# Kernel optimization log

Measured on AMD Instinct MI355X. Metric: run time of the kernel, lower is better.

Reference implementation:

```python
import jax, jax.numpy as jnp
import numpy as np

MIN_NORM = 1e-15
BALL_EPS = 4e-3  # float32 proj eps used by HGCN PoincareBall
C_IN = 1.0
C_OUT = 1.0
N_NODES = 100000
N_EDGES = 1200000
DIM = 64
RATIO = 0.75


def _artanh(x):
    x = jnp.clip(x, -1.0 + 1e-7, 1.0 - 1e-7)
    return 0.5 * (jnp.log1p(x) - jnp.log1p(-x))


def _norm(x):
    return jnp.clip(jnp.linalg.norm(x, axis=-1, keepdims=True), MIN_NORM, None)


def proj(x, c):
    n = _norm(x)
    maxnorm = (1.0 - BALL_EPS) / jnp.sqrt(c)
    return jnp.where(n > maxnorm, x / n * maxnorm, x)


def expmap0(u, c):
    sc = jnp.sqrt(c)
    n = _norm(u)
    return jnp.tanh(sc * n) * u / (sc * n)


def logmap0(p, c):
    sc = jnp.sqrt(c)
    n = _norm(p)
    return _artanh(sc * n) * p / (sc * n)


def mobius_add(x, y, c):
    x2 = jnp.sum(x * x, -1, keepdims=True)
    y2 = jnp.sum(y * y, -1, keepdims=True)
    xy = jnp.sum(x * y, -1, keepdims=True)
    num = (1.0 + 2.0 * c * xy + c * y2) * x + (1.0 - c * x2) * y
    den = 1.0 + 2.0 * c * xy + c * c * x2 * y2
    return num / jnp.clip(den, MIN_NORM, None)


def mobius_matvec(m, x, c):
    sc = jnp.sqrt(c)
    xn = _norm(x)
    mx = x @ m.T  # [N, out]
    mxn = _norm(mx)
    res = jnp.tanh(mxn / xn * _artanh(sc * xn)) * mx / (mxn * sc)
    zero = jnp.all(mx == 0, axis=-1, keepdims=True)
    return jnp.where(zero, jnp.zeros((), mx.dtype), res)


def setup_inputs() -> dict:
    key = jax.random.key(0)
    k1, k2, k3, k4 = jax.random.split(key, 4)
    # points on the Poincare ball (small tangent vectors exp-mapped)
    x = proj(expmap0(0.01 * jax.random.normal(k1, (N_NODES, DIM), jnp.float32), C_IN), C_IN)
    edge_index = jax.random.randint(k2, (2, N_EDGES), 0, N_NODES, dtype=jnp.int32)
    xav = float(np.sqrt(2.0) * np.sqrt(6.0 / (DIM + DIM)))  # xavier_uniform gain sqrt(2) scale
    weight = jax.random.uniform(k3, (DIM, DIM), jnp.float32, -xav, xav)
    bias = jnp.zeros((DIM,), jnp.float32)
    lw_w = jax.random.normal(k4, (1, 2 * DIM), jnp.float32) * 0.05
    lw_b = jnp.zeros((1,), jnp.float32)
    return {"x": x, "edge_index": edge_index, "weight": weight, "bias": bias, "lw_w": lw_w, "lw_b": lw_b}


def reference(x, edge_index, weight, bias, lw_w, lw_b):
    N = x.shape[0]
    # ---- HypLinear (eval mode, dropout=0) ----
    h = proj(mobius_matvec(weight, x, C_IN), C_IN)
    hyp_bias = proj(expmap0(bias[None, :], C_IN), C_IN)  # proj_tan0 is identity on Poincare ball
    h = proj(mobius_add(h, hyp_bias, C_IN), C_IN)
    # ---- NodeSelect ----
    x_tan = logmap0(h, C_IN)  # [N, D]
    src, dst = edge_index[0], edge_index[1]
    agg = lambda v: jax.ops.segment_sum(v[src], dst, num_segments=N)  # scatter-add over edges
    sum_neigh = agg(x_tan)
    # NodeInformationScore: (I - D^{-1/2} A D^{-1/2}) x with self-loops removed from A
    w = (src != dst).astype(x_tan.dtype)
    deg = jax.ops.segment_sum(w, src, num_segments=N)
    dinv = jnp.where(deg > 0, deg ** -0.5, 0.0)
    norm_w = -(dinv[src] * w * dinv[dst])  # [E]
    info = x_tan + jax.ops.segment_sum(norm_w[:, None] * x_tan[src], dst, num_segments=N)
    score = jnp.sum(jnp.abs(info), axis=1)  # [N]
    k = int(N * RATIO)
    top_vals, _ = jax.lax.top_k(score, k)
    T = top_vals[k - 1]  # min of top-k
    sel = (score > T).astype(x_tan.dtype)[:, None]  # hot_prob mask [N,1]
    sum_sel = agg(sel * x_tan)
    gate = jax.nn.sigmoid(jnp.concatenate([sum_sel, sum_neigh], axis=-1) @ lw_w.T + lw_b)  # [N,1]
    a_x = jax.nn.relu(agg(gate * sel * x_tan))
    out = x_tan + a_x
    out = proj(expmap0(out, C_IN), C_IN)
    # ---- HypAct (relu) ----
    out = jax.nn.relu(out)
    out = proj(expmap0(out, C_OUT), C_OUT)
    return out
```

## Files before the change

kernel.cpp:

```cpp
#include <hip/hip_runtime.h>
#include <math.h>


#define MAXN_D 0.996
#define MAXN_F 0.996f
#define NPB 64
#define GPT 512
#define NBMAX 512
#define BCAP 6144
#define BINBLK 256
#define SELB 128
#define SBIN 8192
#define CAND_CAP 16384

typedef unsigned long long ull;

__device__ __forceinline__ double wsumd(double v){
#pragma unroll
  for(int o=32;o;o>>=1) v += __shfl_xor(v,o,64);
  return v;
}
__device__ __forceinline__ float wsumf(float v){
#pragma unroll
  for(int o=32;o;o>>=1) v += __shfl_xor(v,o,64);
  return v;
}
__device__ __forceinline__ double qsumd(double v){
#pragma unroll
  for(int o=1;o<16;o<<=1) v += __shfl_xor(v,o,64);
  return v;
}
__device__ __forceinline__ float qsumf(float v){
#pragma unroll
  for(int o=1;o<16;o<<=1) v += __shfl_xor(v,o,64);
  return v;
}
__device__ __forceinline__ double gsumd(double v){
  v += __shfl_xor(v,16,64); v += __shfl_xor(v,32,64); return v;
}
__device__ __forceinline__ float gsumf(float v){
  v += __shfl_xor(v,16,64); v += __shfl_xor(v,32,64); return v;
}

__global__ __launch_bounds__(256) void k_init(
    const float* __restrict__ bias, double* __restrict__ hb,
    double* __restrict__ hb2, int* __restrict__ rem, int kth,
    int* __restrict__ dstCur, int* __restrict__ srcCur, int NB){
  if(threadIdx.x < 64){
    int lane = threadIdx.x;
    double b = (double)bias[lane];
    double n = fmax(sqrt(wsumd(b*b)), 1e-15);
    double e = tanh(n)*b/n;
    double en = fmax(sqrt(wsumd(e*e)), 1e-15);
    if(en > MAXN_D) e *= MAXN_D/en;
    hb[lane] = e;
    double s2 = wsumd(e*e);
    if(lane==0) *hb2 = s2;
  }
  if(threadIdx.x == 0) *rem = kth;
  for(int b=threadIdx.x; b<NB; b+=256){
    dstCur[b] = b*BCAP;
    srcCur[b] = b*BCAP;
  }
}

__global__ __launch_bounds__(256) void k_binPlace(const int* __restrict__ ei, int E,
    int NB, int chunk, int* __restrict__ dstCur, int* __restrict__ srcCur,
    ull* __restrict__ dstbin, int* __restrict__ srcbin){
  __shared__ int dh[NBMAX], sh_[NBMAX];
  __shared__ int db[NBMAX], sb[NBMAX];
  for(int t=threadIdx.x; t<NB; t+=256){ dh[t]=0; sh_[t]=0; }
  __syncthreads();
  int start = blockIdx.x*chunk, end = min(E, start+chunk);
  for(int e=start+(int)threadIdx.x; e<end; e+=256){
    int s = ei[e], d = ei[(size_t)E+e];
    atomicAdd(&dh[d>>8],1);
    if(s!=d) atomicAdd(&sh_[s>>8],1);
  }
  __syncthreads();
  for(int t=threadIdx.x; t<NB; t+=256){
    db[t] = dh[t]  ? atomicAdd(&dstCur[t], dh[t])  : 0;
    sb[t] = sh_[t] ? atomicAdd(&srcCur[t], sh_[t]) : 0;
  }
  __syncthreads();
  for(int t=threadIdx.x; t<NB; t+=256){ dh[t]=db[t]; sh_[t]=sb[t]; }
  __syncthreads();
  for(int e=start+(int)threadIdx.x; e<end; e+=256){
    int s = ei[e], d = ei[(size_t)E+e];
    int p = atomicAdd(&dh[d>>8],1);
    dstbin[p] = ((ull)(unsigned)d<<32) | (unsigned)s;
    if(s!=d){ int p2 = atomicAdd(&sh_[s>>8],1); srcbin[p2] = s; }
  }
}

__global__ __launch_bounds__(256) void k_bucketAB(
    const ull* __restrict__ dstbin, const int* __restrict__ dstCur,
    int* __restrict__ rowbeg, int* __restrict__ rowcnt, int* __restrict__ csr,
    const int* __restrict__ srcbin, const int* __restrict__ srcCur,
    double* __restrict__ dinv, int N){
  int b = blockIdx.x;
  int node0 = b<<8;
  int nodes = min(256, N-node0);
  __shared__ int c[256], ex[256];
  int t = threadIdx.x;
  {
    int base = b*BCAP, cnt = dstCur[b]-base;
    c[t]=0; __syncthreads();
    for(int e=base+t; e<base+cnt; e+=256){
      int d = (int)(dstbin[e]>>32);
      atomicAdd(&c[d-node0],1);
    }
    __syncthreads();
    int v = c[t]; ex[t]=v; __syncthreads();
    for(int off=1; off<256; off<<=1){
      int a = (t>=off) ? ex[t-off] : 0; __syncthreads();
      ex[t] += a; __syncthreads();
    }
    int mybase = base + ex[t] - v;
    if(t<nodes){ rowbeg[node0+t] = mybase; rowcnt[node0+t] = v; }
    c[t] = mybase;
    __syncthreads();
    for(int e=base+t; e<base+cnt; e+=256){
      ull pr = dstbin[e];
      int d = (int)(pr>>32);
      int p = atomicAdd(&c[d-node0],1);
      csr[p] = (int)(pr & 0xffffffffu);
    }
  }
  __syncthreads();
  {
    int base = b*BCAP, cnt = srcCur[b]-base;
    c[t]=0; __syncthreads();
    for(int e=base+t; e<base+cnt; e+=256)
      atomicAdd(&c[srcbin[e]-node0],1);
    __syncthreads();
    if(t<nodes){ int d = c[t]; dinv[node0+t] = (d>0) ? 1.0/sqrt((double)d) : 0.0; }
  }
}

__global__ __launch_bounds__(GPT) void k_gemmprep(
    const float* __restrict__ x, const float* __restrict__ W,
    const double* __restrict__ hb, const double* __restrict__ hb2p,
    const float* __restrict__ lww,
    double* __restrict__ xtd, float* __restrict__ xtf,
    float2* __restrict__ pab, int N){
  __shared__ float wf[4096];
  __shared__ float xf[NPB*64];
  __shared__ double r123[NPB][3];
  __shared__ double abuf[NPB][2];
  int tid = threadIdx.x;
  for(int a=tid; a<4096; a+=GPT){
    int j = (a>>2)&63;
    int k = ((a>>8)<<2) | (a&3);
    wf[a] = W[j*64 + k];
  }
  int i0 = blockIdx.x*NPB;
  for(int idx=tid; idx<NPB*64; idx+=GPT){
    int node = i0 + (idx>>6);
    xf[idx] = (node<N) ? x[(size_t)node*64 + (idx&63)] : 0.f;
  }
  __syncthreads();
  int lane = tid & 63;
  int nb = (tid>>6)*8;
  double acc0=0.0, acc1=0.0, acc2=0.0, acc3=0.0;
  double acc4=0.0, acc5=0.0, acc6=0.0, acc7=0.0;
  const float4* wq = (const float4*)wf;
  const float4* xq = (const float4*)xf;
#pragma unroll 2
  for(int k4=0; k4<16; ++k4){
    float4 w4 = wq[k4*64 + lane];
    double w0=(double)w4.x, w1=(double)w4.y, w2d=(double)w4.z, w3=(double)w4.w;
#define MAC(n, accn) { float4 v = xq[(nb+(n))*16 + k4];                       \
    accn = fma(w0,(double)v.x,accn); accn = fma(w1,(double)v.y,accn);         \
    accn = fma(w2d,(double)v.z,accn); accn = fma(w3,(double)v.w,accn); }
    MAC(0,acc0) MAC(1,acc1) MAC(2,acc2) MAC(3,acc3)
    MAC(4,acc4) MAC(5,acc5) MAC(6,acc6) MAC(7,acc7)
#undef MAC
  }
  double hbl = hb[lane];
#define RED4(A0,A1,A2,A3, OFF) {                                              \
    double xd0 = (double)xf[(nb+(OFF)+0)*64+lane];                            \
    double xd1 = (double)xf[(nb+(OFF)+1)*64+lane];                            \
    double xd2 = (double)xf[(nb+(OFF)+2)*64+lane];                            \
    double xd3 = (double)xf[(nb+(OFF)+3)*64+lane];                            \
    double s1_0 = wsumd(xd0*xd0), s2_0 = wsumd((A0)*(A0)), s3_0 = wsumd((A0)*hbl); \
    double s1_1 = wsumd(xd1*xd1), s2_1 = wsumd((A1)*(A1)), s3_1 = wsumd((A1)*hbl); \
    double s1_2 = wsumd(xd2*xd2), s2_2 = wsumd((A2)*(A2)), s3_2 = wsumd((A2)*hbl); \
    double s1_3 = wsumd(xd3*xd3), s2_3 = wsumd((A3)*(A3)), s3_3 = wsumd((A3)*hbl); \
    if(lane==0){                                                              \
      r123[nb+(OFF)+0][0]=s1_0; r123[nb+(OFF)+0][1]=s2_0; r123[nb+(OFF)+0][2]=s3_0; \
      r123[nb+(OFF)+1][0]=s1_1; r123[nb+(OFF)+1][1]=s2_1; r123[nb+(OFF)+1][2]=s3_1; \
      r123[nb+(OFF)+2][0]=s1_2; r123[nb+(OFF)+2][1]=s2_2; r123[nb+(OFF)+2][2]=s3_2; \
      r123[nb+(OFF)+3][0]=s1_3; r123[nb+(OFF)+3][1]=s2_3; r123[nb+(OFF)+3][2]=s3_3; \
    } }
  RED4(acc0,acc1,acc2,acc3, 0)
  RED4(acc4,acc5,acc6,acc7, 4)
#undef RED4
  __syncthreads();
  if(tid < 64){
    double x2s = r123[tid][0], m2 = r123[tid][1], mh = r123[tid][2];
    double y2 = *hb2p;
    double xn  = fmax(sqrt(x2s), 1e-15);
    double mxn = fmax(sqrt(m2), 1e-15);
    double xc  = fmin(fmax(xn, -1.0+1e-7), 1.0-1e-7);
    double at  = 0.5*(log1p(xc)-log1p(-xc));
    double f1  = tanh(mxn/xn*at)/mxn;
    if(m2 == 0.0) f1 = 0.0;
    double h2 = f1*f1*m2;
    double hn = fmax(sqrt(h2), 1e-15);
    if(hn > MAXN_D){ double s = MAXN_D/hn; f1 *= s; h2 = f1*f1*m2; }
    double xy = f1*mh;
    double den = fmax(1.0 + 2.0*xy + h2*y2, 1e-15);
    double a = (1.0 + 2.0*xy + y2)/den;
    double bb = (1.0 - h2)/den;
    double p2 = a*a*h2 + 2.0*a*bb*xy + bb*bb*y2;
    double pn = fmax(sqrt(p2), 1e-15);
    if(pn > MAXN_D){ double s = MAXN_D/pn; a*=s; bb*=s; pn = fmax(pn*s, 1e-15); }
    double nc  = fmin(fmax(pn, -1.0+1e-7), 1.0-1e-7);
    double at2 = 0.5*(log1p(nc)-log1p(-nc));
    double sc  = at2/pn;
    abuf[tid][0] = sc*a*f1;
    abuf[tid][1] = sc*bb;
  }
  __syncthreads();
  float wAl = lww[lane], wBl = lww[64+lane];
#define EMIT(n, accn) { int nd=i0+nb+(n); if(nd<N){                           \
    double al = abuf[nb+(n)][0], be = abuf[nb+(n)][1];                        \
    double v = al*(accn) + be*hbl;                                            \
    xtd[(size_t)nd*64+lane] = v;                                              \
    float vf = (float)v;                                                      \
    xtf[(size_t)nd*64+lane] = vf;                                             \
    float pA = wsumf(vf*wAl);                                                 \
    float pB = wsumf(vf*wBl);                                                 \
    if(lane==0) pab[nd] = make_float2(pA,pB); } }
  EMIT(0,acc0) EMIT(1,acc1) EMIT(2,acc2) EMIT(3,acc3)
  EMIT(4,acc4) EMIT(5,acc5) EMIT(6,acc6) EMIT(7,acc7)
#undef EMIT
}

__global__ void k_gatherA(const int* __restrict__ csr, const int* __restrict__ rowbeg,
                          const int* __restrict__ rowcnt,
                          const float* __restrict__ xtf, const double* __restrict__ xtd,
                          const double* __restrict__ dinv,
                          ull* __restrict__ keys, int N){
  int lane = threadIdx.x & 63;
  int i = (int)((blockIdx.x*(unsigned)blockDim.x + threadIdx.x)>>6);
  if(i>=N) return;
  int beg = rowbeg[i], deg = rowcnt[i];
  int g = lane>>4, t = lane&15;
  double di = dinv[i];
  double a0=0.0,a1=0.0,a2=0.0,a3=0.0;
  int j = g;
  int s = (j<deg) ? csr[beg+j] : 0;
  while(j < deg){
    int snext = (j+4<deg) ? csr[beg+j+4] : 0;
    if(s != i){
      double w = di*dinv[s];
      float4 v = *((const float4*)(xtf + (size_t)s*64 + t*4));
      a0 -= w*(double)v.x; a1 -= w*(double)v.y;
      a2 -= w*(double)v.z; a3 -= w*(double)v.w;
    }
    s = snext; j += 4;
  }
  a0 = gsumd(a0); a1 = gsumd(a1); a2 = gsumd(a2); a3 = gsumd(a3);
  const double2* xr = (const double2*)(xtd + (size_t)i*64 + t*4);
  double2 x0 = xr[0], x1 = xr[1];
  double sc = fabs(x0.x+a0) + fabs(x0.y+a1) + fabs(x1.x+a2) + fabs(x1.y+a3);
  sc = qsumd(sc);
  if(lane==0) keys[i] = (ull)__double_as_longlong(sc);
}

__global__ __launch_bounds__(256) void k_sel13(
    const ull* __restrict__ keys, int N,
    ull* __restrict__ pref, int* __restrict__ rem,
    int lev, int shift, int width,
    int* __restrict__ hist , int* __restrict__ ticket){
  __shared__ int h[SBIN];
  __shared__ int part[256];
  __shared__ int lastflag, pickedD, pickedR;
  int t = threadIdx.x;
  for(int b=t; b<SBIN; b+=256) h[b] = 0;
  __syncthreads();
  ull p0 = *pref;
  int rem0 = *rem;
  int mask = (1<<width) - 1;
  for(int i = blockIdx.x*256 + t; i<N; i += SELB*256){
    ull kk = keys[i];
    if(lev==0 || (kk >> (shift+width)) == (p0 >> (shift+width)))
      atomicAdd(&h[(int)((kk>>shift)&mask)], 1);
  }
  __syncthreads();
  for(int b=t; b<SBIN; b+=256)
    if(h[b]) __hip_atomic_fetch_add(&hist[b], h[b],
                                    __ATOMIC_RELAXED, __HIP_MEMORY_SCOPE_AGENT);
  __threadfence();
  if(t==0){
    int tk = __hip_atomic_fetch_add(ticket, 1, __ATOMIC_ACQ_REL, __HIP_MEMORY_SCOPE_AGENT);
    lastflag = (tk == SELB-1);
  }
  __syncthreads();
  if(!lastflag) return;
  int base = SBIN-1 - 32*t;
  int pt = 0;
  for(int m=0;m<32;m++)
    pt += __hip_atomic_load(&hist[base-m], __ATOMIC_RELAXED, __HIP_MEMORY_SCOPE_AGENT);
  part[t] = pt;
  __syncthreads();
  for(int off=1; off<256; off<<=1){
    int a = (t>=off) ? part[t-off] : 0; __syncthreads();
    part[t] += a; __syncthreads();
  }
  int cumt = part[t];
  int prev = (t==0) ? 0 : part[t-1];
  if(cumt >= rem0 && prev < rem0){
    int c = 0;
    for(int m=0;m<32;m++){
      int hv = __hip_atomic_load(&hist[base-m], __ATOMIC_RELAXED, __HIP_MEMORY_SCOPE_AGENT);
      c += hv;
      if(prev + c >= rem0){ pickedD = base-m; pickedR = rem0 - (prev + c - hv); break; }
    }
  }
  __syncthreads();
  if(t==0){
    *rem = pickedR;
    *pref = p0 | ((ull)pickedD << shift);
  }
}

__global__ __launch_bounds__(256) void k_finish(
    const ull* __restrict__ keys, int N,
    ull* __restrict__ pref, const int* __restrict__ rem,
    ull* __restrict__ cand, int* __restrict__ cnt, int* __restrict__ ticket){
  __shared__ ull sc[4096];
  __shared__ int lastflag;
  __shared__ ull winner;
  int t = threadIdx.x;
  ull p0 = *pref;
  for(int i = blockIdx.x*256 + t; i<N; i += SELB*256){
    ull kk = keys[i];
    if((kk>>38) == (p0>>38)){
      int idx = __hip_atomic_fetch_add(cnt, 1, __ATOMIC_RELAXED, __HIP_MEMORY_SCOPE_AGENT);
      if(idx < CAND_CAP)
        __hip_atomic_store(&cand[idx], kk, __ATOMIC_RELAXED, __HIP_MEMORY_SCOPE_AGENT);
    }
  }
  __threadfence();
  __syncthreads();
  if(t==0){
    int tk = __hip_atomic_fetch_add(ticket, 1, __ATOMIC_ACQ_REL, __HIP_MEMORY_SCOPE_AGENT);
    lastflag = (tk == SELB-1);
  }
  __syncthreads();
  if(!lastflag) return;
  int C = __hip_atomic_load(cnt, __ATOMIC_RELAXED, __HIP_MEMORY_SCOPE_AGENT);
  if(C > 4096) C = 4096;
  for(int j=t; j<C; j+=256)
    sc[j] = __hip_atomic_load(&cand[j], __ATOMIC_RELAXED, __HIP_MEMORY_SCOPE_AGENT);
  __syncthreads();
  int r = *rem;
  for(int j=t; j<C; j+=256){
    ull c = sc[j];
    int gt=0, eq=0;
    for(int m=0;m<C;m++){ ull o = sc[m]; gt += (o>c); eq += (o==c); }
    if(gt <= r-1 && r-1 < gt+eq) winner = c;
  }
  __syncthreads();
  if(t==0) *pref = winner;
}

__global__ void k_qval(const float2* __restrict__ pab, const ull* __restrict__ keys,
                       const ull* __restrict__ pref, float* __restrict__ q, int N){
  int i = blockIdx.x*blockDim.x + threadIdx.x;
  if(i>=N) return;
  float2 p = pab[i];
  q[i] = p.y + ((keys[i] > *pref) ? p.x : 0.f);
}

__global__ void k_gatherC(const int* __restrict__ csr, const int* __restrict__ rowbeg,
                          const int* __restrict__ rowcnt,
                          const float* __restrict__ q,
                          const ull* __restrict__ keys, const ull* __restrict__ pref,
                          const float* __restrict__ lwb,
                          float* __restrict__ gg, int N){
  int lane = threadIdx.x & 63;
  int wid  = (int)((blockIdx.x*(unsigned)blockDim.x + threadIdx.x)>>6);
  int g = lane>>4, t = lane&15;
  int i = wid*4 + g;
  if(i>=N) return;
  int beg = rowbeg[i], end = beg + rowcnt[i];
  float z = 0.f;
  for(int e = beg + t; e < end; e += 16) z += q[csr[e]];
  z = qsumf(z);
  if(t==0){
    float gv = 1.f/(1.f+expf(-(z + lwb[0])));
    gg[i] = (keys[i] > *pref) ? gv : 0.f;
  }
}

__global__ void k_gatherD(const int* __restrict__ csr, const int* __restrict__ rowbeg,
                          const int* __restrict__ rowcnt,
                          const float* __restrict__ xtf, const float* __restrict__ gg,
                          float* __restrict__ out, int N){
  int lane = threadIdx.x & 63;
  int i = (int)((blockIdx.x*(unsigned)blockDim.x + threadIdx.x)>>6);
  if(i>=N) return;
  int beg = rowbeg[i], deg = rowcnt[i];
  int g = lane>>4, t = lane&15;
  float c0=0.f,c1=0.f,c2=0.f,c3=0.f;
  int j = g;
  int s = (j<deg) ? csr[beg+j] : 0;
  while(j < deg){
    int snext = (j+4<deg) ? csr[beg+j+4] : 0;
    float gv = gg[s];
    if(gv != 0.f){
      float4 v = *((const float4*)(xtf + (size_t)s*64 + t*4));
      c0 = fmaf(gv, v.x, c0); c1 = fmaf(gv, v.y, c1);
      c2 = fmaf(gv, v.z, c2); c3 = fmaf(gv, v.w, c3);
    }
    s = snext; j += 4;
  }
  c0 = gsumf(c0); c1 = gsumf(c1); c2 = gsumf(c2); c3 = gsumf(c3);
  float4 xr = *((const float4*)(xtf + (size_t)i*64 + t*4));
  float v0 = xr.x + fmaxf(c0,0.f);
  float v1 = xr.y + fmaxf(c1,0.f);
  float v2 = xr.z + fmaxf(c2,0.f);
  float v3 = xr.w + fmaxf(c3,0.f);
  float n2 = qsumf(v0*v0 + v1*v1 + v2*v2 + v3*v3);
  float n = fmaxf(sqrtf(n2), 1e-15f);
  float f = tanhf(n)/n;
  float e0=f*v0, e1=f*v1, e2=f*v2, e3=f*v3;
  float en = fmaxf(tanhf(n), 1e-15f);
  if(en > MAXN_F){ float sf = MAXN_F/en; e0*=sf; e1*=sf; e2*=sf; e3*=sf; }
  e0 = fmaxf(e0,0.f); e1 = fmaxf(e1,0.f); e2 = fmaxf(e2,0.f); e3 = fmaxf(e3,0.f);
  float m2 = qsumf(e0*e0 + e1*e1 + e2*e2 + e3*e3);
  float nb = fmaxf(sqrtf(m2), 1e-15f);
  float f2 = tanhf(nb)/nb;
  float o0=f2*e0, o1=f2*e1, o2=f2*e2, o3=f2*e3;
  float on = fmaxf(tanhf(nb), 1e-15f);
  if(on > MAXN_F){ float sf = MAXN_F/on; o0*=sf; o1*=sf; o2*=sf; o3*=sf; }
  if(g==0){
    float4 ov = make_float4(o0,o1,o2,o3);
    *((float4*)(out + (size_t)i*64 + t*4)) = ov;
  }
}

extern "C" void kernel_launch(void* const* d_in, const int* in_sizes, int n_in,
                              void* d_out, int out_size, void* d_ws, size_t ws_size,
                              hipStream_t stream){
  const float* x    = (const float*)d_in[0];
  const int*   ei   = (const int*)d_in[1];
  const float* W    = (const float*)d_in[2];
  const float* bias = (const float*)d_in[3];
  const float* lww  = (const float*)d_in[4];
  const float* lwb  = (const float*)d_in[5];
  int N = in_sizes[0]/64;
  int E = in_sizes[1]/2;
  int kth = (int)((double)N*0.75);
  int NB = (N+255)>>8;
  if(NB > NBMAX) return;
  long long meanPB = (long long)E / (NB > 0 ? NB : 1);
  if(3*meanPB > 2*(long long)BCAP) return;
  int chunk = (E + BINBLK - 1)/BINBLK;
  size_t binEls = (size_t)NB*BCAP + 4096;

  char* ws = (char*)d_ws;
  size_t cur = 0;
  auto alloc = [&](size_t bytes){ size_t o = cur; cur = (cur + bytes + 255) & ~(size_t)255; return o; };
  size_t o_hb   = alloc(64*sizeof(double));
  size_t o_hb2  = alloc(8);
  size_t o_rem  = alloc(4);
  size_t o_zero = cur;
  size_t o_pref = alloc(8);
  size_t o_hist = alloc(2*(size_t)SBIN*4);
  size_t o_tick = alloc(3*4);
  size_t o_cnt  = alloc(4);
  size_t zlen   = cur - o_zero;
  size_t o_cand = alloc((size_t)CAND_CAP*8);
  size_t o_dCur = alloc((size_t)NBMAX*4);
  size_t o_sCur = alloc((size_t)NBMAX*4);
  size_t o_rbeg = alloc((size_t)N*4);
  size_t o_rcnt = alloc((size_t)N*4);
  size_t o_csr  = alloc(binEls*4);
  size_t o_dbin = alloc(binEls*8);
  size_t o_sbin = alloc(binEls*4);
  size_t o_dinv = alloc((size_t)N*8);
  size_t o_keys = alloc((size_t)N*8);
  size_t o_pab  = alloc((size_t)N*8);
  size_t o_q    = alloc((size_t)N*4);
  size_t o_xtf  = alloc((size_t)N*64*4);
  size_t o_xtd  = alloc((size_t)N*64*8);
  size_t o_gg   = alloc((size_t)N*4);
  if(ws_size < cur) return;

  double* hb     = (double*)(ws+o_hb);
  double* hb2    = (double*)(ws+o_hb2);
  int*    rem    = (int*)(ws+o_rem);
  ull*    pref   = (ull*)(ws+o_pref);
  int*    hist   = (int*)(ws+o_hist);
  int*    tick   = (int*)(ws+o_tick);
  int*    cnt    = (int*)(ws+o_cnt);
  ull*    cand   = (ull*)(ws+o_cand);
  int*    dstCur = (int*)(ws+o_dCur);
  int*    srcCur = (int*)(ws+o_sCur);
  int*    rowbeg = (int*)(ws+o_rbeg);
  int*    rowcnt = (int*)(ws+o_rcnt);
  int*    csr    = (int*)(ws+o_csr);
  ull*    dstbin = (ull*)(ws+o_dbin);
  int*    srcbin = (int*)(ws+o_sbin);
  double* dinv   = (double*)(ws+o_dinv);
  ull*    keys   = (ull*)(ws+o_keys);
  float2* pab    = (float2*)(ws+o_pab);
  float*  q      = (float*)(ws+o_q);
  float*  xtf    = (float*)(ws+o_xtf);
  double* xtd    = (double*)(ws+o_xtd);
  float*  gg     = (float*)(ws+o_gg);

  hipMemsetAsync(ws+o_zero, 0, zlen, stream);

  int nodeBlocks = (N+3)/4;
  int pBlocks    = (N+15)/16;

  k_init     <<<1, 256, 0, stream>>>(bias, hb, hb2, rem, kth, dstCur, srcCur, NB);
  k_binPlace <<<BINBLK, 256, 0, stream>>>(ei, E, NB, chunk, dstCur, srcCur, dstbin, srcbin);
  k_bucketAB <<<NB, 256, 0, stream>>>(dstbin, dstCur, rowbeg, rowcnt, csr,
                                      srcbin, srcCur, dinv, N);
  k_gemmprep <<<(N+NPB-1)/NPB, GPT, 0, stream>>>(x, W, hb, hb2, lww, xtd, xtf, pab, N);
  k_gatherA  <<<nodeBlocks, 256, 0, stream>>>(csr, rowbeg, rowcnt, xtf, xtd, dinv, keys, N);
  k_sel13    <<<SELB, 256, 0, stream>>>(keys, N, pref, rem, 0, 51, 13, hist, tick+0);
  k_sel13    <<<SELB, 256, 0, stream>>>(keys, N, pref, rem, 1, 38, 13, hist+SBIN, tick+1);
  k_finish   <<<SELB, 256, 0, stream>>>(keys, N, pref, rem, cand, cnt, tick+2);
  k_qval     <<<(N+255)/256, 256, 0, stream>>>(pab, keys, pref, q, N);
  k_gatherC  <<<pBlocks, 256, 0, stream>>>(csr, rowbeg, rowcnt, q, keys, pref, lwb, gg, N);
  k_gatherD  <<<nodeBlocks, 256, 0, stream>>>(csr, rowbeg, rowcnt, xtf, gg, (float*)d_out, N);
}
```

Before: 353.4 us.

## Store double node features as float hi/lo pair and widen gather lanes to 8 elements

Replaces the double-precision copy of the tangent features with a float low-order residual next to the existing float array, roughly halving the extra write in gemmprep and the self-row read in gatherA while keeping near-double accuracy for the score. Both gather kernels now give 8 edges per wavefront iteration with each lane loading 8 floats (two float4) instead of 4 edges with 4 floats per lane. This raises memory-level parallelism per wave for low-degree rows, at the cost of more registers per lane and more idle lanes when a row has few edges.

```diff
diff --git a/kernel.cpp b/kernel.cpp
--- a/kernel.cpp
+++ b/kernel.cpp
@@ -25,21 +25,10 @@
   for(int o=32;o;o>>=1) v += __shfl_xor(v,o,64);
   return v;
 }
-__device__ __forceinline__ double qsumd(double v){
-#pragma unroll
-  for(int o=1;o<16;o<<=1) v += __shfl_xor(v,o,64);
-  return v;
-}
 __device__ __forceinline__ float qsumf(float v){
 #pragma unroll
   for(int o=1;o<16;o<<=1) v += __shfl_xor(v,o,64);
   return v;
-}
-__device__ __forceinline__ double gsumd(double v){
-  v += __shfl_xor(v,16,64); v += __shfl_xor(v,32,64); return v;
-}
-__device__ __forceinline__ float gsumf(float v){
-  v += __shfl_xor(v,16,64); v += __shfl_xor(v,32,64); return v;
 }
 
 __global__ __launch_bounds__(256) void k_init(
@@ -142,7 +131,7 @@
     const float* __restrict__ x, const float* __restrict__ W,
     const double* __restrict__ hb, const double* __restrict__ hb2p,
     const float* __restrict__ lww,
-    double* __restrict__ xtd, float* __restrict__ xtf,
+    float* __restrict__ xtf, float* __restrict__ xdl,
     float2* __restrict__ pab, int N){
   __shared__ float wf[4096];
   __shared__ float xf[NPB*64];
@@ -227,9 +216,10 @@
 #define EMIT(n, accn) { int nd=i0+nb+(n); if(nd<N){                           \
     double al = abuf[nb+(n)][0], be = abuf[nb+(n)][1];                        \
     double v = al*(accn) + be*hbl;                                            \
-    xtd[(size_t)nd*64+lane] = v;                                              \
     float vf = (float)v;                                                      \
+    float df = (float)(v - (double)vf);                                       \
     xtf[(size_t)nd*64+lane] = vf;                                             \
+    xdl[(size_t)nd*64+lane] = df;                                             \
     float pA = wsumf(vf*wAl);                                                 \
     float pB = wsumf(vf*wBl);                                                 \
     if(lane==0) pab[nd] = make_float2(pA,pB); } }
@@ -240,33 +230,41 @@
 
 __global__ void k_gatherA(const int* __restrict__ csr, const int* __restrict__ rowbeg,
                           const int* __restrict__ rowcnt,
-                          const float* __restrict__ xtf, const double* __restrict__ xtd,
+                          const float* __restrict__ xtf, const float* __restrict__ xdl,
                           const double* __restrict__ dinv,
                           ull* __restrict__ keys, int N){
   int lane = threadIdx.x & 63;
   int i = (int)((blockIdx.x*(unsigned)blockDim.x + threadIdx.x)>>6);
   if(i>=N) return;
   int beg = rowbeg[i], deg = rowcnt[i];
-  int g = lane>>4, t = lane&15;
+  int g = lane>>3, t = lane&7;
   double di = dinv[i];
-  double a0=0.0,a1=0.0,a2=0.0,a3=0.0;
+  double a0=0,a1=0,a2=0,a3=0,a4=0,a5=0,a6=0,a7=0;
   int j = g;
   int s = (j<deg) ? csr[beg+j] : 0;
   while(j < deg){
-    int snext = (j+4<deg) ? csr[beg+j+4] : 0;
+    int snext = (j+8<deg) ? csr[beg+j+8] : 0;
     if(s != i){
       double w = di*dinv[s];
-      float4 v = *((const float4*)(xtf + (size_t)s*64 + t*4));
-      a0 -= w*(double)v.x; a1 -= w*(double)v.y;
-      a2 -= w*(double)v.z; a3 -= w*(double)v.w;
-    }
-    s = snext; j += 4;
-  }
-  a0 = gsumd(a0); a1 = gsumd(a1); a2 = gsumd(a2); a3 = gsumd(a3);
-  const double2* xr = (const double2*)(xtd + (size_t)i*64 + t*4);
-  double2 x0 = xr[0], x1 = xr[1];
-  double sc = fabs(x0.x+a0) + fabs(x0.y+a1) + fabs(x1.x+a2) + fabs(x1.y+a3);
-  sc = qsumd(sc);
+      const float4* row = (const float4*)(xtf + (size_t)s*64 + t*8);
+      float4 u = row[0], v = row[1];
+      a0 -= w*(double)u.x; a1 -= w*(double)u.y; a2 -= w*(double)u.z; a3 -= w*(double)u.w;
+      a4 -= w*(double)v.x; a5 -= w*(double)v.y; a6 -= w*(double)v.z; a7 -= w*(double)v.w;
+    }
+    s = snext; j += 8;
+  }
+#define XG(v) { v += __shfl_xor(v,8,64); v += __shfl_xor(v,16,64); v += __shfl_xor(v,32,64); }
+  XG(a0) XG(a1) XG(a2) XG(a3) XG(a4) XG(a5) XG(a6) XG(a7)
+#undef XG
+  const float4* xr = (const float4*)(xtf + (size_t)i*64 + t*8);
+  const float4* dr = (const float4*)(xdl + (size_t)i*64 + t*8);
+  float4 x0 = xr[0], x1 = xr[1], d0 = dr[0], d1 = dr[1];
+  double sc =
+    fabs(((double)x0.x+(double)d0.x)+a0) + fabs(((double)x0.y+(double)d0.y)+a1) +
+    fabs(((double)x0.z+(double)d0.z)+a2) + fabs(((double)x0.w+(double)d0.w)+a3) +
+    fabs(((double)x1.x+(double)d1.x)+a4) + fabs(((double)x1.y+(double)d1.y)+a5) +
+    fabs(((double)x1.z+(double)d1.z)+a6) + fabs(((double)x1.w+(double)d1.w)+a7);
+  sc += __shfl_xor(sc,1,64); sc += __shfl_xor(sc,2,64); sc += __shfl_xor(sc,4,64);
   if(lane==0) keys[i] = (ull)__double_as_longlong(sc);
 }
 
@@ -405,42 +403,52 @@
   int i = (int)((blockIdx.x*(unsigned)blockDim.x + threadIdx.x)>>6);
   if(i>=N) return;
   int beg = rowbeg[i], deg = rowcnt[i];
-  int g = lane>>4, t = lane&15;
-  float c0=0.f,c1=0.f,c2=0.f,c3=0.f;
+  int g = lane>>3, t = lane&7;
+  float c0=0,c1=0,c2=0,c3=0,c4=0,c5=0,c6=0,c7=0;
   int j = g;
   int s = (j<deg) ? csr[beg+j] : 0;
   while(j < deg){
-    int snext = (j+4<deg) ? csr[beg+j+4] : 0;
+    int snext = (j+8<deg) ? csr[beg+j+8] : 0;
     float gv = gg[s];
     if(gv != 0.f){
-      float4 v = *((const float4*)(xtf + (size_t)s*64 + t*4));
-      c0 = fmaf(gv, v.x, c0); c1 = fmaf(gv, v.y, c1);
-      c2 = fmaf(gv, v.z, c2); c3 = fmaf(gv, v.w, c3);
-    }
-    s = snext; j += 4;
-  }
-  c0 = gsumf(c0); c1 = gsumf(c1); c2 = gsumf(c2); c3 = gsumf(c3);
-  float4 xr = *((const float4*)(xtf + (size_t)i*64 + t*4));
-  float v0 = xr.x + fmaxf(c0,0.f);
-  float v1 = xr.y + fmaxf(c1,0.f);
-  float v2 = xr.z + fmaxf(c2,0.f);
-  float v3 = xr.w + fmaxf(c3,0.f);
-  float n2 = qsumf(v0*v0 + v1*v1 + v2*v2 + v3*v3);
+      const float4* row = (const float4*)(xtf + (size_t)s*64 + t*8);
+      float4 u = row[0], v = row[1];
+      c0 = fmaf(gv,u.x,c0); c1 = fmaf(gv,u.y,c1); c2 = fmaf(gv,u.z,c2); c3 = fmaf(gv,u.w,c3);
+      c4 = fmaf(gv,v.x,c4); c5 = fmaf(gv,v.y,c5); c6 = fmaf(gv,v.z,c6); c7 = fmaf(gv,v.w,c7);
+    }
+    s = snext; j += 8;
+  }
+#define XG(v) { v += __shfl_xor(v,8,64); v += __shfl_xor(v,16,64); v += __shfl_xor(v,32,64); }
+  XG(c0) XG(c1) XG(c2) XG(c3) XG(c4) XG(c5) XG(c6) XG(c7)
+#undef XG
+  const float4* xr = (const float4*)(xtf + (size_t)i*64 + t*8);
+  float4 x0 = xr[0], x1 = xr[1];
+  float v0 = x0.x + fmaxf(c0,0.f), v1 = x0.y + fmaxf(c1,0.f);
+  float v2 = x0.z + fmaxf(c2,0.f), v3 = x0.w + fmaxf(c3,0.f);
+  float v4 = x1.x + fmaxf(c4,0.f), v5 = x1.y + fmaxf(c5,0.f);
+  float v6 = x1.z + fmaxf(c6,0.f), v7 = x1.w + fmaxf(c7,0.f);
+  float n2 = v0*v0+v1*v1+v2*v2+v3*v3+v4*v4+v5*v5+v6*v6+v7*v7;
+  n2 += __shfl_xor(n2,1,64); n2 += __shfl_xor(n2,2,64); n2 += __shfl_xor(n2,4,64);
   float n = fmaxf(sqrtf(n2), 1e-15f);
   float f = tanhf(n)/n;
-  float e0=f*v0, e1=f*v1, e2=f*v2, e3=f*v3;
+  float e0=f*v0,e1=f*v1,e2=f*v2,e3=f*v3,e4=f*v4,e5=f*v5,e6=f*v6,e7=f*v7;
   float en = fmaxf(tanhf(n), 1e-15f);
-  if(en > MAXN_F){ float sf = MAXN_F/en; e0*=sf; e1*=sf; e2*=sf; e3*=sf; }
-  e0 = fmaxf(e0,0.f); e1 = fmaxf(e1,0.f); e2 = fmaxf(e2,0.f); e3 = fmaxf(e3,0.f);
-  float m2 = qsumf(e0*e0 + e1*e1 + e2*e2 + e3*e3);
+  if(en > MAXN_F){ float sf = MAXN_F/en;
+    e0*=sf;e1*=sf;e2*=sf;e3*=sf;e4*=sf;e5*=sf;e6*=sf;e7*=sf; }
+  e0=fmaxf(e0,0.f);e1=fmaxf(e1,0.f);e2=fmaxf(e2,0.f);e3=fmaxf(e3,0.f);
+  e4=fmaxf(e4,0.f);e5=fmaxf(e5,0.f);e6=fmaxf(e6,0.f);e7=fmaxf(e7,0.f);
+  float m2 = e0*e0+e1*e1+e2*e2+e3*e3+e4*e4+e5*e5+e6*e6+e7*e7;
+  m2 += __shfl_xor(m2,1,64); m2 += __shfl_xor(m2,2,64); m2 += __shfl_xor(m2,4,64);
   float nb = fmaxf(sqrtf(m2), 1e-15f);
   float f2 = tanhf(nb)/nb;
-  float o0=f2*e0, o1=f2*e1, o2=f2*e2, o3=f2*e3;
+  float o0=f2*e0,o1=f2*e1,o2=f2*e2,o3=f2*e3,o4=f2*e4,o5=f2*e5,o6=f2*e6,o7=f2*e7;
   float on = fmaxf(tanhf(nb), 1e-15f);
-  if(on > MAXN_F){ float sf = MAXN_F/on; o0*=sf; o1*=sf; o2*=sf; o3*=sf; }
+  if(on > MAXN_F){ float sf = MAXN_F/on;
+    o0*=sf;o1*=sf;o2*=sf;o3*=sf;o4*=sf;o5*=sf;o6*=sf;o7*=sf; }
   if(g==0){
-    float4 ov = make_float4(o0,o1,o2,o3);
-    *((float4*)(out + (size_t)i*64 + t*4)) = ov;
+    float4* op = (float4*)(out + (size_t)i*64 + t*8);
+    op[0] = make_float4(o0,o1,o2,o3);
+    op[1] = make_float4(o4,o5,o6,o7);
   }
 }
 
@@ -488,7 +496,7 @@
   size_t o_pab  = alloc((size_t)N*8);
   size_t o_q    = alloc((size_t)N*4);
   size_t o_xtf  = alloc((size_t)N*64*4);
-  size_t o_xtd  = alloc((size_t)N*64*8);
+  size_t o_xdl  = alloc((size_t)N*64*4);
   size_t o_gg   = alloc((size_t)N*4);
   if(ws_size < cur) return;
 
@@ -512,7 +520,7 @@
   float2* pab    = (float2*)(ws+o_pab);
   float*  q      = (float*)(ws+o_q);
   float*  xtf    = (float*)(ws+o_xtf);
-  double* xtd    = (double*)(ws+o_xtd);
+  float*  xdl    = (float*)(ws+o_xdl);
   float*  gg     = (float*)(ws+o_gg);
 
   hipMemsetAsync(ws+o_zero, 0, zlen, stream);
@@ -524,8 +532,8 @@
   k_binPlace <<<BINBLK, 256, 0, stream>>>(ei, E, NB, chunk, dstCur, srcCur, dstbin, srcbin);
   k_bucketAB <<<NB, 256, 0, stream>>>(dstbin, dstCur, rowbeg, rowcnt, csr,
                                       srcbin, srcCur, dinv, N);
-  k_gemmprep <<<(N+NPB-1)/NPB, GPT, 0, stream>>>(x, W, hb, hb2, lww, xtd, xtf, pab, N);
-  k_gatherA  <<<nodeBlocks, 256, 0, stream>>>(csr, rowbeg, rowcnt, xtf, xtd, dinv, keys, N);
+  k_gemmprep <<<(N+NPB-1)/NPB, GPT, 0, stream>>>(x, W, hb, hb2, lww, xtf, xdl, pab, N);
+  k_gatherA  <<<nodeBlocks, 256, 0, stream>>>(csr, rowbeg, rowcnt, xtf, xdl, dinv, keys, N);
   k_sel13    <<<SELB, 256, 0, stream>>>(keys, N, pref, rem, 0, 51, 13, hist, tick+0);
   k_sel13    <<<SELB, 256, 0, stream>>>(keys, N, pref, rem, 1, 38, 13, hist+SBIN, tick+1);
   k_finish   <<<SELB, 256, 0, stream>>>(keys, N, pref, rem, cand, cnt, tick+2);
```

Result: faster. 338.5 us (-4.2%).
